# Kernel tuning notes

Hardware: AMD Instinct MI355X
Metric: run time of the kernel (lower is better)

The kernel has to match this reference:

```python
import jax, jax.numpy as jnp
import numpy as np

N = 100000          # nodes
E = 1600000         # edges (before self-loops)
F_IN = 128          # dataset.num_node_features
HID = 32            # hidden_channels
HEADS = 4
NUM_CLASSES = 40
NEG_SLOPE = 0.2     # PyG GATConv default


def setup_inputs() -> dict:
    key = jax.random.key(0)
    ks = jax.random.split(key, 16)
    x = jax.random.normal(ks[0], (N, F_IN), dtype=jnp.float32)
    edge_index = jax.random.randint(ks[1], (2, E), 0, N, dtype=jnp.int64)

    def glorot(k, shape):
        lim = float(np.sqrt(6.0 / (shape[0] + shape[-1])))
        return jax.random.uniform(k, shape, jnp.float32, -lim, lim)

    # layer 0: F_IN -> HID, heads=HEADS, concat
    W0 = glorot(ks[2], (F_IN, HEADS * HID))
    as0 = glorot(ks[3], (HEADS, HID))
    ad0 = glorot(ks[4], (HEADS, HID))
    b0 = jnp.zeros((HEADS * HID,), jnp.float32)
    # layer 1: HEADS*HID -> HID, heads=HEADS, concat
    W1 = glorot(ks[5], (HEADS * HID, HEADS * HID))
    as1 = glorot(ks[6], (HEADS, HID))
    ad1 = glorot(ks[7], (HEADS, HID))
    b1 = jnp.zeros((HEADS * HID,), jnp.float32)
    # layer 2: HEADS*HID -> HID, heads=1, no concat
    W2 = glorot(ks[8], (HEADS * HID, HID))
    as2 = glorot(ks[9], (1, HID))
    ad2 = glorot(ks[10], (1, HID))
    b2 = jnp.zeros((HID,), jnp.float32)
    # final linear HID -> NUM_CLASSES
    lin_w = glorot(ks[11], (HID, NUM_CLASSES))
    lin_b = jnp.zeros((NUM_CLASSES,), jnp.float32)
    return dict(x=x, edge_index=edge_index, W0=W0, as0=as0, ad0=ad0, b0=b0,
                W1=W1, as1=as1, ad1=ad1, b1=b1,
                W2=W2, as2=as2, ad2=ad2, b2=b2, lin_w=lin_w, lin_b=lin_b)


def gat_conv(x, src, dst, W, a_src, a_dst, b, heads, out_ch, concat):
    n = x.shape[0]
    h = (x @ W).reshape(n, heads, out_ch)               # [N,H,C]
    alpha_s = (h * a_src).sum(-1)                        # [N,H]
    alpha_d = (h * a_dst).sum(-1)                        # [N,H]
    e = jax.nn.leaky_relu(alpha_s[src] + alpha_d[dst], NEG_SLOPE)  # [E,H]
    m = jax.ops.segment_max(e, dst, num_segments=n)      # segment softmax over in-edges
    e = jnp.exp(e - m[dst])
    denom = jax.ops.segment_sum(e, dst, num_segments=n)
    alpha = e / (denom[dst] + 1e-16)                     # [E,H]
    out = jax.ops.segment_sum(h[src] * alpha[:, :, None], dst, num_segments=n)  # [N,H,C]
    out = out.reshape(n, heads * out_ch) if concat else out.mean(axis=1)
    return out + b


def reference(x, edge_index, W0, as0, ad0, b0, W1, as1, ad1, b1,
              W2, as2, ad2, b2, lin_w, lin_b):
    n = x.shape[0]
    loop = jnp.arange(n, dtype=edge_index.dtype)
    src = jnp.concatenate([edge_index[0], loop])   # PyG GATConv adds self-loops
    dst = jnp.concatenate([edge_index[1], loop])
    x = jax.nn.relu(gat_conv(x, src, dst, W0, as0, ad0, b0, HEADS, HID, True))
    x = jax.nn.relu(gat_conv(x, src, dst, W1, as1, ad1, b1, HEADS, HID, True))
    x = jax.nn.relu(gat_conv(x, src, dst, W2, as2, ad2, b2, 1, HID, False))
    return x @ lin_w + lin_b
```

## Files before the change

kernel.cpp:

```cpp
#include <hip/hip_runtime.h>
#include <hip/hip_bf16.h>
#include <hip/hip_fp16.h>
#include <math.h>


#define NEG_SLOPE 0.2f

typedef __attribute__((ext_vector_type(8))) _Float16 f16x8;
typedef __attribute__((ext_vector_type(4))) float    f32x4;


__global__ void zero1_kernel(int* __restrict__ a, int n) {
    int i = blockIdx.x * blockDim.x + threadIdx.x;
    if (i < n) a[i] = 0;
}

__global__ void count_rank_kernel(const int* __restrict__ ei, int eraw, int n,
                                  int* __restrict__ deg, int* __restrict__ rank) {
    int i = blockIdx.x * blockDim.x + threadIdx.x;
    int etot = eraw + n;
    if (i >= etot) return;
    int dst = (i < eraw) ? ei[eraw + i] : (i - eraw);
    rank[i] = atomicAdd(&deg[dst], 1);
}

__global__ __launch_bounds__(1024)
void scan_local_kernel(const int* __restrict__ deg, int* __restrict__ rowptr,
                       int* __restrict__ bsum, int n) {
    __shared__ int buf[1024];
    int tid = threadIdx.x;
    int i = blockIdx.x * 1024 + tid;
    int v = (i < n) ? deg[i] : 0;
    buf[tid] = v;
    __syncthreads();
    for (int off = 1; off < 1024; off <<= 1) {
        int t = (tid >= off) ? buf[tid - off] : 0;
        __syncthreads();
        buf[tid] += t;
        __syncthreads();
    }
    if (i < n) rowptr[i] = buf[tid] - v;
    if (tid == 1023) bsum[blockIdx.x] = buf[1023];
}

__global__ __launch_bounds__(128)
void scan_sums_kernel(const int* __restrict__ bsum, int* __restrict__ boffs, int nb) {
    __shared__ int buf[128];
    int tid = threadIdx.x;
    int v = (tid < nb) ? bsum[tid] : 0;
    buf[tid] = v;
    __syncthreads();
    for (int off = 1; off < 128; off <<= 1) {
        int t = (tid >= off) ? buf[tid - off] : 0;
        __syncthreads();
        buf[tid] += t;
        __syncthreads();
    }
    if (tid < nb) boffs[tid] = buf[tid] - v;
}

__global__ void scan_add_kernel(int* __restrict__ rowptr, const int* __restrict__ boffs,
                                int n, int etot) {
    int i = blockIdx.x * blockDim.x + threadIdx.x;
    if (i < n) rowptr[i] += boffs[i >> 10];
    if (i == 0) rowptr[n] = etot;
}

__global__ void scatter2_kernel(const int* __restrict__ ei, const int* __restrict__ rank,
                                int eraw, int n, const int* __restrict__ rowptr,
                                int* __restrict__ csr_src) {
    int i = blockIdx.x * blockDim.x + threadIdx.x;
    int etot = eraw + n;
    if (i >= etot) return;
    int src, dst;
    if (i < eraw) { src = ei[i]; dst = ei[eraw + i]; }
    else          { src = i - eraw; dst = src; }
    csr_src[rowptr[dst] + rank[i]] = src;
}


__global__ void wpack_f16_kernel(const float* __restrict__ W, __half* __restrict__ Wp) {
    int i = blockIdx.x * blockDim.x + threadIdx.x;
    int j    = i & 7;
    int lane = (i >> 3) & 63;
    int ks   = (i >> 9) & 3;
    int ct   = i >> 11;
    int k = ks * 32 + (lane >> 4) * 8 + j;
    int c = ct * 16 + (lane & 15);
    Wp[i] = __float2half(W[k * 128 + c]);
}


template <bool F32IN>
__global__ __launch_bounds__(256)
void gemm_mfma_coef_kernel(const void* __restrict__ Xv, const __half* __restrict__ Wp,
                           const float* __restrict__ a_s, const float* __restrict__ a_d,
                           __half* __restrict__ H, float* __restrict__ as_out,
                           float* __restrict__ ad_out, int n) {
    int t = threadIdx.x;
    int wave = t >> 6, lane = t & 63;
    int l15 = lane & 15;
    int kg  = lane >> 4;
    int base = blockIdx.x * 128 + wave * 32;

    int row0 = base + l15;
    int row1 = base + 16 + l15;
    int r0c = (row0 < n) ? row0 : 0;
    int r1c = (row1 < n) ? row1 : 0;

    f32x4 acc[2][8];
#pragma unroll
    for (int tt = 0; tt < 2; tt++)
#pragma unroll
        for (int i = 0; i < 8; i++) acc[tt][i] = (f32x4){0.f, 0.f, 0.f, 0.f};

#pragma unroll
    for (int ks = 0; ks < 4; ks++) {
        f16x8 a0, a1;
        if constexpr (F32IN) {
            const float* X = (const float*)Xv;
            const float* p0 = X + (size_t)r0c * 128 + kg * 8 + ks * 32;
            const float* p1 = X + (size_t)r1c * 128 + kg * 8 + ks * 32;
            float4 x0 = *(const float4*)(p0), x1 = *(const float4*)(p0 + 4);
            a0[0] = (_Float16)x0.x; a0[1] = (_Float16)x0.y; a0[2] = (_Float16)x0.z; a0[3] = (_Float16)x0.w;
            a0[4] = (_Float16)x1.x; a0[5] = (_Float16)x1.y; a0[6] = (_Float16)x1.z; a0[7] = (_Float16)x1.w;
            float4 y0 = *(const float4*)(p1), y1 = *(const float4*)(p1 + 4);
            a1[0] = (_Float16)y0.x; a1[1] = (_Float16)y0.y; a1[2] = (_Float16)y0.z; a1[3] = (_Float16)y0.w;
            a1[4] = (_Float16)y1.x; a1[5] = (_Float16)y1.y; a1[6] = (_Float16)y1.z; a1[7] = (_Float16)y1.w;
        } else {
            const __half* X = (const __half*)Xv;
            a0 = *(const f16x8*)(X + (size_t)r0c * 128 + kg * 8 + ks * 32);
            a1 = *(const f16x8*)(X + (size_t)r1c * 128 + kg * 8 + ks * 32);
        }
#pragma unroll
        for (int ct = 0; ct < 8; ct++) {
            f16x8 b = *(const f16x8*)(Wp + (size_t)((ct * 4 + ks) * 64 + lane) * 8);
            acc[0][ct] = __builtin_amdgcn_mfma_f32_16x16x32_f16(a0, b, acc[0][ct], 0, 0, 0);
            acc[1][ct] = __builtin_amdgcn_mfma_f32_16x16x32_f16(a1, b, acc[1][ct], 0, 0, 0);
        }
    }

#pragma unroll
    for (int tt = 0; tt < 2; tt++) {
#pragma unroll
        for (int ct = 0; ct < 8; ct++) {
#pragma unroll
            for (int r = 0; r < 4; r++) {
                int orow = base + tt * 16 + kg * 4 + r;
                if (orow < n)
                    H[(size_t)orow * 128 + ct * 16 + l15] = __float2half(acc[tt][ct][r]);
            }
        }
    }

#pragma unroll
    for (int h = 0; h < 4; h++) {
        float ws0 = a_s[h * 32 + l15];
        float ws1 = a_s[h * 32 + 16 + l15];
        float wd0 = a_d[h * 32 + l15];
        float wd1 = a_d[h * 32 + 16 + l15];
#pragma unroll
        for (int tt = 0; tt < 2; tt++) {
#pragma unroll
            for (int r = 0; r < 4; r++) {
                float v0 = acc[tt][2 * h][r];
                float v1 = acc[tt][2 * h + 1][r];
                float ps = v0 * ws0 + v1 * ws1;
                float pd = v0 * wd0 + v1 * wd1;
                ps += __shfl_xor(ps, 1, 16); pd += __shfl_xor(pd, 1, 16);
                ps += __shfl_xor(ps, 2, 16); pd += __shfl_xor(pd, 2, 16);
                ps += __shfl_xor(ps, 4, 16); pd += __shfl_xor(pd, 4, 16);
                ps += __shfl_xor(ps, 8, 16); pd += __shfl_xor(pd, 8, 16);
                int orow = base + tt * 16 + kg * 4 + r;
                if (l15 == 0 && orow < n) {
                    as_out[(size_t)orow * 4 + h] = ps;
                    ad_out[(size_t)orow * 4 + h] = pd;
                }
            }
        }
    }
}


__global__ __launch_bounds__(128)
void gemm_l2_f16_kernel(const __half* __restrict__ X, const float* __restrict__ W,
                        __half* __restrict__ H, int n) {
    __shared__ float xs[8][129];
    int base = blockIdx.x * 8;
    int tid = threadIdx.x;
#pragma unroll
    for (int it = 0; it < 4; it++) {
        int i = tid + it * 128;
        int r = i >> 6, c2 = i & 63;
        int row = base + r;
        __half2 v = (row < n) ? ((const __half2*)(X + (size_t)row * 128))[c2]
                              : __floats2half2_rn(0.f, 0.f);
        float2 f = __half22float2(v);
        xs[r][c2 * 2] = f.x; xs[r][c2 * 2 + 1] = f.y;
    }
    __syncthreads();
    int col  = tid & 31;
    int rsub = tid >> 5;
    float acc0 = 0.f, acc1 = 0.f;
    for (int k = 0; k < 128; k++) {
        float w = W[k * 32 + col];
        acc0 += xs[rsub][k] * w;
        acc1 += xs[rsub + 4][k] * w;
    }
    int row0 = base + rsub;
    if (row0 < n)     H[(size_t)row0 * 32 + col]       = __float2half(acc0);
    if (row0 + 4 < n) H[(size_t)(row0 + 4) * 32 + col] = __float2half(acc1);
}

__global__ void attn_coef_l2_f16_kernel(const __half* __restrict__ H,
                                        const float* __restrict__ a_s,
                                        const float* __restrict__ a_d,
                                        float* __restrict__ as_out,
                                        float* __restrict__ ad_out, int n) {
    int i = blockIdx.x * blockDim.x + threadIdx.x;
    if (i >= n) return;
    const __half2* hp = (const __half2*)(H + (size_t)i * 32);
    float s = 0.f, d = 0.f;
#pragma unroll
    for (int c2 = 0; c2 < 16; c2++) {
        float2 v = __half22float2(hp[c2]);
        s += v.x * a_s[2 * c2] + v.y * a_s[2 * c2 + 1];
        d += v.x * a_d[2 * c2] + v.y * a_d[2 * c2 + 1];
    }
    as_out[i] = s;
    ad_out[i] = d;
}


struct h4pack { __half2 a, b; };

__global__ __launch_bounds__(256)
void gat_fused_f16_kernel(const __half* __restrict__ Hm,
                          const float* __restrict__ as_,
                          const float* __restrict__ ad_,
                          const int* __restrict__ rowptr,
                          const int* __restrict__ csr,
                          const float* __restrict__ bias,
                          __half* __restrict__ out, int n) {
    constexpr int GS = 32;
    int t = threadIdx.x;
    int node = blockIdx.x * 8 + (t >> 5);
    if (node >= n) return;
    int tl = t & 31;
    int h  = tl >> 3;
    int k8 = tl & 7;
    const uint2* H8 = (const uint2*)Hm;
    int e0 = rowptr[node], e1 = rowptr[node + 1];
    float ad_d = ad_[(size_t)node * 4 + h];

    int  ce  = e0 + k8;
    bool vA  = ce < e1;
    int  idxA = vA ? csr[ce] : 0;
    float asA = vA ? as_[(size_t)idxA * 4 + h] : 0.f;

    float m = -INFINITY, l = 0.f;
    float4 acc = make_float4(0.f, 0.f, 0.f, 0.f);

    for (int eb = e0; eb < e1; eb += 8) {
        uint2 u[8];
#pragma unroll
        for (int j = 0; j < 8; j++) {
            int src = __shfl(idxA, j, 8);
            u[j] = H8[(size_t)src * GS + tl];
        }

        int  ne  = eb + 8 + k8;
        bool vB  = ne < e1;
        int  idxB = vB ? csr[ne] : 0;
        float asB = vB ? as_[(size_t)idxB * 4 + h] : 0.f;

        float el = asA + ad_d;
        el = (el > 0.f) ? el : NEG_SLOPE * el;
        el = vA ? el : -INFINITY;

        float cm = el;
        cm = fmaxf(cm, __shfl_xor(cm, 1, 8));
        cm = fmaxf(cm, __shfl_xor(cm, 2, 8));
        cm = fmaxf(cm, __shfl_xor(cm, 4, 8));
        float m_new = fmaxf(m, cm);
        float scale = __expf(m - m_new);
        float p = vA ? __expf(el - m_new) : 0.f;

        float ps = p;
        ps += __shfl_xor(ps, 1, 8);
        ps += __shfl_xor(ps, 2, 8);
        ps += __shfl_xor(ps, 4, 8);
        l = l * scale + ps;
        acc.x *= scale; acc.y *= scale; acc.z *= scale; acc.w *= scale;
        m = m_new;

#pragma unroll
        for (int j = 0; j < 8; j++) {
            float pj  = __shfl(p, j, 8);
            float2 f01 = __half22float2(*(const __half2*)&u[j].x);
            float2 f23 = __half22float2(*(const __half2*)&u[j].y);
            acc.x += pj * f01.x; acc.y += pj * f01.y;
            acc.z += pj * f23.x; acc.w += pj * f23.y;
        }
        idxA = idxB; asA = asB; vA = vB;
    }

    float li = 1.f / (l + 1e-16f);
    float4 b4 = ((const float4*)bias)[tl];
    float4 o;
    o.x = fmaxf(acc.x * li + b4.x, 0.f);
    o.y = fmaxf(acc.y * li + b4.y, 0.f);
    o.z = fmaxf(acc.z * li + b4.z, 0.f);
    o.w = fmaxf(acc.w * li + b4.w, 0.f);
    h4pack po;
    po.a = __floats2half2_rn(o.x, o.y);
    po.b = __floats2half2_rn(o.z, o.w);
    ((h4pack*)out)[(size_t)node * 32 + tl] = po;
}


__global__ __launch_bounds__(256)
void gat_fused_l2_kernel(const __half* __restrict__ Hm,
                         const float* __restrict__ as_,
                         const float* __restrict__ ad_,
                         const int* __restrict__ rowptr,
                         const int* __restrict__ csr,
                         const float* __restrict__ bias,
                         const float* __restrict__ lw,
                         const float* __restrict__ lb,
                         float* __restrict__ out, int n) {
    int t = threadIdx.x;
    int node = blockIdx.x * 32 + (t >> 3);
    if (node >= n) return;
    int tl = t & 7;
    const uint2* H8 = (const uint2*)Hm;
    int e0 = rowptr[node], e1 = rowptr[node + 1];
    float ad_d = ad_[node];

    int  ce  = e0 + tl;
    bool vA  = ce < e1;
    int  idxA = vA ? csr[ce] : 0;
    float asA = vA ? as_[idxA] : 0.f;

    float m = -INFINITY, l = 0.f;
    float4 acc = make_float4(0.f, 0.f, 0.f, 0.f);

    for (int eb = e0; eb < e1; eb += 8) {
        uint2 u[8];
#pragma unroll
        for (int j = 0; j < 8; j++) {
            int src = __shfl(idxA, j, 8);
            u[j] = H8[(size_t)src * 8 + tl];
        }

        int  ne  = eb + 8 + tl;
        bool vB  = ne < e1;
        int  idxB = vB ? csr[ne] : 0;
        float asB = vB ? as_[idxB] : 0.f;

        float el = asA + ad_d;
        el = (el > 0.f) ? el : NEG_SLOPE * el;
        el = vA ? el : -INFINITY;

        float cm = el;
        cm = fmaxf(cm, __shfl_xor(cm, 1, 8));
        cm = fmaxf(cm, __shfl_xor(cm, 2, 8));
        cm = fmaxf(cm, __shfl_xor(cm, 4, 8));
        float m_new = fmaxf(m, cm);
        float scale = __expf(m - m_new);
        float p = vA ? __expf(el - m_new) : 0.f;

        float ps = p;
        ps += __shfl_xor(ps, 1, 8);
        ps += __shfl_xor(ps, 2, 8);
        ps += __shfl_xor(ps, 4, 8);
        l = l * scale + ps;
        acc.x *= scale; acc.y *= scale; acc.z *= scale; acc.w *= scale;
        m = m_new;

#pragma unroll
        for (int j = 0; j < 8; j++) {
            float pj  = __shfl(p, j, 8);
            float2 f01 = __half22float2(*(const __half2*)&u[j].x);
            float2 f23 = __half22float2(*(const __half2*)&u[j].y);
            acc.x += pj * f01.x; acc.y += pj * f01.y;
            acc.z += pj * f23.x; acc.w += pj * f23.y;
        }
        idxA = idxB; asA = asB; vA = vB;
    }

    float li = 1.f / (l + 1e-16f);
    float4 b4 = ((const float4*)bias)[tl];
    float4 o;
    o.x = fmaxf(acc.x * li + b4.x, 0.f);
    o.y = fmaxf(acc.y * li + b4.y, 0.f);
    o.z = fmaxf(acc.z * li + b4.z, 0.f);
    o.w = fmaxf(acc.w * li + b4.w, 0.f);

    float fin0 = lb[tl];
    float fin1 = lb[tl + 8];
    float fin2 = lb[tl + 16];
    float fin3 = lb[tl + 24];
    float fin4 = lb[tl + 32];
#pragma unroll
    for (int j = 0; j < 8; j++) {
        float vx = __shfl(o.x, j, 8);
        float vy = __shfl(o.y, j, 8);
        float vz = __shfl(o.z, j, 8);
        float vw = __shfl(o.w, j, 8);
        const float* l0 = lw + (size_t)(4 * j) * 40;
#pragma unroll
        for (int c = 0; c < 5; c++) {
            int cls = tl + 8 * c;
            float v = vx * l0[cls] + vy * l0[40 + cls] + vz * l0[80 + cls] + vw * l0[120 + cls];
            if (c == 0) fin0 += v;
            else if (c == 1) fin1 += v;
            else if (c == 2) fin2 += v;
            else if (c == 3) fin3 += v;
            else fin4 += v;
        }
    }
    float* op = out + (size_t)node * 40;
    op[tl]      = fin0;
    op[tl + 8]  = fin1;
    op[tl + 16] = fin2;
    op[tl + 24] = fin3;
    op[tl + 32] = fin4;
}


extern "C" void kernel_launch(void* const* d_in, const int* in_sizes, int n_in,
                              void* d_out, int out_size, void* d_ws, size_t ws_size,
                              hipStream_t stream) {
    const float* x   = (const float*)d_in[0];
    const int*   ei  = (const int*)d_in[1];
    const float* W0  = (const float*)d_in[2];
    const float* as0 = (const float*)d_in[3];
    const float* ad0 = (const float*)d_in[4];
    const float* b0  = (const float*)d_in[5];
    const float* W1  = (const float*)d_in[6];
    const float* as1 = (const float*)d_in[7];
    const float* ad1 = (const float*)d_in[8];
    const float* b1  = (const float*)d_in[9];
    const float* W2  = (const float*)d_in[10];
    const float* as2 = (const float*)d_in[11];
    const float* ad2 = (const float*)d_in[12];
    const float* b2  = (const float*)d_in[13];
    const float* lw  = (const float*)d_in[14];
    const float* lb  = (const float*)d_in[15];
    float* out = (float*)d_out;

    const int n    = in_sizes[0] / 128;
    const int eraw = in_sizes[1] / 2;
    const int etot = eraw + n;
    const int nb   = (n + 1023) / 1024;

    char* wsp = (char*)d_ws;
    size_t off = 0;
    auto alloc = [&](size_t bytes) -> void* {
        void* p = wsp + off;
        off += (bytes + 255) & ~(size_t)255;
        return p;
    };
    __half* h16    = (__half*)alloc((size_t)n * 128 * 2);
    __half* buf16  = (__half*)alloc((size_t)n * 128 * 2);
    __half* h2     = (__half*)alloc((size_t)n * 32 * 2);
    __half* Wp0    = (__half*)alloc((size_t)128 * 128 * 2);
    __half* Wp1    = (__half*)alloc((size_t)128 * 128 * 2);
    float*  asb    = (float*)alloc((size_t)n * 4 * 4);
    float*  adb    = (float*)alloc((size_t)n * 4 * 4);
    int*    deg    = (int*)alloc((size_t)n * 4);
    int*    rank   = (int*)alloc((size_t)etot * 4);
    int*    rowptr = (int*)alloc((size_t)(n + 1) * 4);
    int*    csr    = (int*)alloc((size_t)etot * 4);
    int*    bsum   = (int*)alloc((size_t)nb * 4);
    int*    boffs  = (int*)alloc((size_t)nb * 4);

    zero1_kernel<<<(n + 255) / 256, 256, 0, stream>>>(deg, n);
    count_rank_kernel<<<(etot + 255) / 256, 256, 0, stream>>>(ei, eraw, n, deg, rank);
    wpack_f16_kernel<<<64, 256, 0, stream>>>(W0, Wp0);
    wpack_f16_kernel<<<64, 256, 0, stream>>>(W1, Wp1);
    scan_local_kernel<<<nb, 1024, 0, stream>>>(deg, rowptr, bsum, n);
    scan_sums_kernel<<<1, 128, 0, stream>>>(bsum, boffs, nb);
    scan_add_kernel<<<(n + 255) / 256, 256, 0, stream>>>(rowptr, boffs, n, etot);
    scatter2_kernel<<<(etot + 255) / 256, 256, 0, stream>>>(ei, rank, eraw, n, rowptr, csr);

    const int gblocks = (n + 127) / 128;

    gemm_mfma_coef_kernel<true><<<gblocks, 256, 0, stream>>>(x, Wp0, as0, ad0, h16, asb, adb, n);
    gat_fused_f16_kernel<<<(n + 7) / 8, 256, 0, stream>>>(h16, asb, adb, rowptr, csr, b0, buf16, n);

    gemm_mfma_coef_kernel<false><<<gblocks, 256, 0, stream>>>(buf16, Wp1, as1, ad1, h16, asb, adb, n);
    gat_fused_f16_kernel<<<(n + 7) / 8, 256, 0, stream>>>(h16, asb, adb, rowptr, csr, b1, buf16, n);

    gemm_l2_f16_kernel<<<(n + 7) / 8, 128, 0, stream>>>(buf16, W2, h2, n);
    attn_coef_l2_f16_kernel<<<(n + 255) / 256, 256, 0, stream>>>(h2, as2, ad2, asb, adb, n);
    gat_fused_l2_kernel<<<(n + 31) / 32, 256, 0, stream>>>(h2, asb, adb, rowptr, csr, b2, lw, lb, out, n);
}
```

Before: 501.1 us.

## Stage GEMM outputs through LDS and fuse layer-2 GEMM with MFMA and attention coefficients

After: 466.7 us. 1.07x faster.

```diff
diff --git a/kernel.cpp b/kernel.cpp
--- a/kernel.cpp
+++ b/kernel.cpp
@@ -79,6 +79,7 @@
 }
 
 
+template <int OUTC>
 __global__ void wpack_f16_kernel(const float* __restrict__ W, __half* __restrict__ Wp) {
     int i = blockIdx.x * blockDim.x + threadIdx.x;
     int j    = i & 7;
@@ -87,7 +88,7 @@
     int ct   = i >> 11;
     int k = ks * 32 + (lane >> 4) * 8 + j;
     int c = ct * 16 + (lane & 15);
-    Wp[i] = __float2half(W[k * 128 + c]);
+    Wp[i] = __float2half(W[k * OUTC + c]);
 }
 
 
@@ -97,14 +98,15 @@
                            const float* __restrict__ a_s, const float* __restrict__ a_d,
                            __half* __restrict__ H, float* __restrict__ as_out,
                            float* __restrict__ ad_out, int n) {
+    __shared__ __half hs[4][32][136];
     int t = threadIdx.x;
     int wave = t >> 6, lane = t & 63;
     int l15 = lane & 15;
     int kg  = lane >> 4;
-    int base = blockIdx.x * 128 + wave * 32;
-
-    int row0 = base + l15;
-    int row1 = base + 16 + l15;
+    int wbase = blockIdx.x * 128 + wave * 32;
+
+    int row0 = wbase + l15;
+    int row1 = wbase + 16 + l15;
     int r0c = (row0 < n) ? row0 : 0;
     int r1c = (row1 < n) ? row1 : 0;
 
@@ -141,94 +143,119 @@
     }
 
 #pragma unroll
-    for (int tt = 0; tt < 2; tt++) {
-#pragma unroll
-        for (int ct = 0; ct < 8; ct++) {
-#pragma unroll
-            for (int r = 0; r < 4; r++) {
-                int orow = base + tt * 16 + kg * 4 + r;
-                if (orow < n)
-                    H[(size_t)orow * 128 + ct * 16 + l15] = __float2half(acc[tt][ct][r]);
+    for (int tt = 0; tt < 2; tt++)
+#pragma unroll
+        for (int ct = 0; ct < 8; ct++)
+#pragma unroll
+            for (int r = 0; r < 4; r++)
+                hs[wave][tt * 16 + kg * 4 + r][ct * 16 + l15] = __float2half(acc[tt][ct][r]);
+    __syncthreads();
+
+#pragma unroll
+    for (int it = 0; it < 8; it++) {
+        int lr    = it * 4 + (lane >> 4);
+        int chunk = lane & 15;
+        int orow  = wbase + lr;
+        if (orow < n) {
+            uint4 v = *(const uint4*)&hs[wave][lr][chunk * 8];
+            *(uint4*)(H + (size_t)orow * 128 + chunk * 8) = v;
+        }
+    }
+
+    {
+        int row = lane & 31;
+        int hh  = lane >> 5;
+        int orow = wbase + row;
+        if (orow < n) {
+#pragma unroll
+            for (int hi = 0; hi < 2; hi++) {
+                int h = hh + 2 * hi;
+                const __half2* hp = (const __half2*)&hs[wave][row][h * 32];
+                float s = 0.f, d = 0.f;
+#pragma unroll
+                for (int c2 = 0; c2 < 16; c2++) {
+                    float2 v = __half22float2(hp[c2]);
+                    s += v.x * a_s[h * 32 + 2 * c2] + v.y * a_s[h * 32 + 2 * c2 + 1];
+                    d += v.x * a_d[h * 32 + 2 * c2] + v.y * a_d[h * 32 + 2 * c2 + 1];
+                }
+                as_out[(size_t)orow * 4 + h] = s;
+                ad_out[(size_t)orow * 4 + h] = d;
             }
         }
     }
-
-#pragma unroll
-    for (int h = 0; h < 4; h++) {
-        float ws0 = a_s[h * 32 + l15];
-        float ws1 = a_s[h * 32 + 16 + l15];
-        float wd0 = a_d[h * 32 + l15];
-        float wd1 = a_d[h * 32 + 16 + l15];
-#pragma unroll
-        for (int tt = 0; tt < 2; tt++) {
-#pragma unroll
-            for (int r = 0; r < 4; r++) {
-                float v0 = acc[tt][2 * h][r];
-                float v1 = acc[tt][2 * h + 1][r];
-                float ps = v0 * ws0 + v1 * ws1;
-                float pd = v0 * wd0 + v1 * wd1;
-                ps += __shfl_xor(ps, 1, 16); pd += __shfl_xor(pd, 1, 16);
-                ps += __shfl_xor(ps, 2, 16); pd += __shfl_xor(pd, 2, 16);
-                ps += __shfl_xor(ps, 4, 16); pd += __shfl_xor(pd, 4, 16);
-                ps += __shfl_xor(ps, 8, 16); pd += __shfl_xor(pd, 8, 16);
-                int orow = base + tt * 16 + kg * 4 + r;
-                if (l15 == 0 && orow < n) {
-                    as_out[(size_t)orow * 4 + h] = ps;
-                    ad_out[(size_t)orow * 4 + h] = pd;
-                }
+}
+
+
+__global__ __launch_bounds__(256)
+void gemm_mfma_l2_kernel(const __half* __restrict__ X, const __half* __restrict__ Wp,
+                         const float* __restrict__ a_s, const float* __restrict__ a_d,
+                         __half* __restrict__ H, float* __restrict__ as_out,
+                         float* __restrict__ ad_out, int n) {
+    __shared__ __half hs[4][32][40];
+    int t = threadIdx.x;
+    int wave = t >> 6, lane = t & 63;
+    int l15 = lane & 15;
+    int kg  = lane >> 4;
+    int wbase = blockIdx.x * 128 + wave * 32;
+
+    int row0 = wbase + l15;
+    int row1 = wbase + 16 + l15;
+    int r0c = (row0 < n) ? row0 : 0;
+    int r1c = (row1 < n) ? row1 : 0;
+
+    f32x4 acc[2][2];
+#pragma unroll
+    for (int tt = 0; tt < 2; tt++)
+#pragma unroll
+        for (int i = 0; i < 2; i++) acc[tt][i] = (f32x4){0.f, 0.f, 0.f, 0.f};
+
+#pragma unroll
+    for (int ks = 0; ks < 4; ks++) {
+        f16x8 a0 = *(const f16x8*)(X + (size_t)r0c * 128 + kg * 8 + ks * 32);
+        f16x8 a1 = *(const f16x8*)(X + (size_t)r1c * 128 + kg * 8 + ks * 32);
+#pragma unroll
+        for (int ct = 0; ct < 2; ct++) {
+            f16x8 b = *(const f16x8*)(Wp + (size_t)((ct * 4 + ks) * 64 + lane) * 8);
+            acc[0][ct] = __builtin_amdgcn_mfma_f32_16x16x32_f16(a0, b, acc[0][ct], 0, 0, 0);
+            acc[1][ct] = __builtin_amdgcn_mfma_f32_16x16x32_f16(a1, b, acc[1][ct], 0, 0, 0);
+        }
+    }
+
+#pragma unroll
+    for (int tt = 0; tt < 2; tt++)
+#pragma unroll
+        for (int ct = 0; ct < 2; ct++)
+#pragma unroll
+            for (int r = 0; r < 4; r++)
+                hs[wave][tt * 16 + kg * 4 + r][ct * 16 + l15] = __float2half(acc[tt][ct][r]);
+    __syncthreads();
+
+#pragma unroll
+    for (int it = 0; it < 2; it++) {
+        int lr    = it * 16 + (lane >> 2);
+        int chunk = lane & 3;
+        int orow  = wbase + lr;
+        if (orow < n) {
+            uint4 v = *(const uint4*)&hs[wave][lr][chunk * 8];
+            *(uint4*)(H + (size_t)orow * 32 + chunk * 8) = v;
+        }
+    }
+
+    if (lane < 32) {
+        int orow = wbase + lane;
+        if (orow < n) {
+            const __half2* hp = (const __half2*)&hs[wave][lane][0];
+            float s = 0.f, d = 0.f;
+#pragma unroll
+            for (int c2 = 0; c2 < 16; c2++) {
+                float2 v = __half22float2(hp[c2]);
+                s += v.x * a_s[2 * c2] + v.y * a_s[2 * c2 + 1];
+                d += v.x * a_d[2 * c2] + v.y * a_d[2 * c2 + 1];
             }
-        }
-    }
-}
-
-
-__global__ __launch_bounds__(128)
-void gemm_l2_f16_kernel(const __half* __restrict__ X, const float* __restrict__ W,
-                        __half* __restrict__ H, int n) {
-    __shared__ float xs[8][129];
-    int base = blockIdx.x * 8;
-    int tid = threadIdx.x;
-#pragma unroll
-    for (int it = 0; it < 4; it++) {
-        int i = tid + it * 128;
-        int r = i >> 6, c2 = i & 63;
-        int row = base + r;
-        __half2 v = (row < n) ? ((const __half2*)(X + (size_t)row * 128))[c2]
-                              : __floats2half2_rn(0.f, 0.f);
-        float2 f = __half22float2(v);
-        xs[r][c2 * 2] = f.x; xs[r][c2 * 2 + 1] = f.y;
-    }
-    __syncthreads();
-    int col  = tid & 31;
-    int rsub = tid >> 5;
-    float acc0 = 0.f, acc1 = 0.f;
-    for (int k = 0; k < 128; k++) {
-        float w = W[k * 32 + col];
-        acc0 += xs[rsub][k] * w;
-        acc1 += xs[rsub + 4][k] * w;
-    }
-    int row0 = base + rsub;
-    if (row0 < n)     H[(size_t)row0 * 32 + col]       = __float2half(acc0);
-    if (row0 + 4 < n) H[(size_t)(row0 + 4) * 32 + col] = __float2half(acc1);
-}
-
-__global__ void attn_coef_l2_f16_kernel(const __half* __restrict__ H,
-                                        const float* __restrict__ a_s,
-                                        const float* __restrict__ a_d,
-                                        float* __restrict__ as_out,
-                                        float* __restrict__ ad_out, int n) {
-    int i = blockIdx.x * blockDim.x + threadIdx.x;
-    if (i >= n) return;
-    const __half2* hp = (const __half2*)(H + (size_t)i * 32);
-    float s = 0.f, d = 0.f;
-#pragma unroll
-    for (int c2 = 0; c2 < 16; c2++) {
-        float2 v = __half22float2(hp[c2]);
-        s += v.x * a_s[2 * c2] + v.y * a_s[2 * c2 + 1];
-        d += v.x * a_d[2 * c2] + v.y * a_d[2 * c2 + 1];
-    }
-    as_out[i] = s;
-    ad_out[i] = d;
+            as_out[orow] = s;
+            ad_out[orow] = d;
+        }
+    }
 }
 
 
@@ -467,6 +494,7 @@
     __half* h2     = (__half*)alloc((size_t)n * 32 * 2);
     __half* Wp0    = (__half*)alloc((size_t)128 * 128 * 2);
     __half* Wp1    = (__half*)alloc((size_t)128 * 128 * 2);
+    __half* Wp2    = (__half*)alloc((size_t)128 * 32 * 2);
     float*  asb    = (float*)alloc((size_t)n * 4 * 4);
     float*  adb    = (float*)alloc((size_t)n * 4 * 4);
     int*    deg    = (int*)alloc((size_t)n * 4);
@@ -478,8 +506,9 @@
 
     zero1_kernel<<<(n + 255) / 256, 256, 0, stream>>>(deg, n);
     count_rank_kernel<<<(etot + 255) / 256, 256, 0, stream>>>(ei, eraw, n, deg, rank);
-    wpack_f16_kernel<<<64, 256, 0, stream>>>(W0, Wp0);
-    wpack_f16_kernel<<<64, 256, 0, stream>>>(W1, Wp1);
+    wpack_f16_kernel<128><<<64, 256, 0, stream>>>(W0, Wp0);
+    wpack_f16_kernel<128><<<64, 256, 0, stream>>>(W1, Wp1);
+    wpack_f16_kernel<32><<<16, 256, 0, stream>>>(W2, Wp2);
     scan_local_kernel<<<nb, 1024, 0, stream>>>(deg, rowptr, bsum, n);
     scan_sums_kernel<<<1, 128, 0, stream>>>(bsum, boffs, nb);
     scan_add_kernel<<<(n + 255) / 256, 256, 0, stream>>>(rowptr, boffs, n, etot);
@@ -493,7 +522,6 @@
     gemm_mfma_coef_kernel<false><<<gblocks, 256, 0, stream>>>(buf16, Wp1, as1, ad1, h16, asb, adb, n);
     gat_fused_f16_kernel<<<(n + 7) / 8, 256, 0, stream>>>(h16, asb, adb, rowptr, csr, b1, buf16, n);
 
-    gemm_l2_f16_kernel<<<(n + 7) / 8, 128, 0, stream>>>(buf16, W2, h2, n);
-    attn_coef_l2_f16_kernel<<<(n + 255) / 256, 256, 0, stream>>>(h2, as2, ad2, asb, adb, n);
+    gemm_mfma_l2_kernel<<<gblocks, 256, 0, stream>>>(buf16, Wp2, as2, ad2, h2, asb, adb, n);
     gat_fused_l2_kernel<<<(n + 31) / 32, 256, 0, stream>>>(h2, asb, adb, rowptr, csr, b2, lw, lb, out, n);
 }
```
